# Optimization experiments

Hardware: AMD Instinct MI355X
Metric: run time of the kernel (lower is better)

## Reference

```python
import jax, jax.numpy as jnp
import numpy as np

EMBED_DIM = 1024
NUM_HEADS = 16
HEAD_DIM = EMBED_DIM // NUM_HEADS


def setup_inputs() -> dict:
    key = jax.random.key(0)
    ks = jax.random.split(key, 7)
    B, S, E = 2, 2048, EMBED_DIM
    scale = 1.0 / np.sqrt(E)
    x = jax.random.normal(ks[0], (B, S, E), dtype=jnp.float32)
    Wq = jax.random.normal(ks[1], (E, E), dtype=jnp.float32) * scale
    Wk = jax.random.normal(ks[2], (E, E), dtype=jnp.float32) * scale
    Wv = jax.random.normal(ks[3], (E, E), dtype=jnp.float32) * scale
    bq = jax.random.normal(ks[4], (E,), dtype=jnp.float32) * 0.01
    bk = jax.random.normal(ks[5], (E,), dtype=jnp.float32) * 0.01
    bv = jax.random.normal(ks[6], (E,), dtype=jnp.float32) * 0.01
    return {"x": x, "Wq": Wq, "bq": bq, "Wk": Wk, "bk": bk, "Wv": Wv, "bv": bv}


def reference(x, Wq, bq, Wk, bk, Wv, bv):
    B, S, E = x.shape
    H, D = NUM_HEADS, HEAD_DIM
    # QKV projections (nn.Linear: x @ W^T + b; W sampled square so we use x @ W + b equivalently as the learned map)
    q = (x @ Wq + bq).reshape(B, S, H, D)
    k = (x @ Wk + bk).reshape(B, S, H, D)
    v = (x @ Wv + bv).reshape(B, S, H, D)
    # scores: [B, H, S, S] -- NOTE: original applies no 1/sqrt(d) scaling
    scores = jnp.einsum("bqhd,bkhd->bhqk", q, k)
    attn = jax.nn.softmax(scores, axis=-1)
    out = jnp.einsum("bhqk,bkhd->bqhd", attn, v)
    return out.reshape(B, S, E)
```

## Files before the change

kernel.cpp:

```cpp
#include <hip/hip_runtime.h>

#define E_DIM 1024
#define NHEADS 16
#define HDIM 64
#define BATCH 2
#define SEQ 2048
#define M_TOT (BATCH*SEQ)

typedef _Float16 f16;
typedef _Float16 half4 __attribute__((ext_vector_type(4)));
typedef _Float16 half8 __attribute__((ext_vector_type(8)));
typedef _Float16 half2v __attribute__((ext_vector_type(2)));
typedef float floatx4 __attribute__((ext_vector_type(4)));

#define MFMA16x32(a,b,c) __builtin_amdgcn_mfma_f32_16x16x32_f16((a),(b),(c),0,0,0)
#define EXP2F(x) __builtin_amdgcn_exp2f(x)
#define FMAX3(a,b,c) fmaxf(fmaxf((a),(b)),(c))

__device__ __forceinline__ half2v pkrtz(float a, float b) {
    return __builtin_bit_cast(half2v, __builtin_amdgcn_cvt_pkrtz(a, b));
}

__device__ __forceinline__ void gll16(const f16* gsrc, f16* ldst) {
    __builtin_amdgcn_global_load_lds(
        (const __attribute__((address_space(1))) void*)gsrc,
        (__attribute__((address_space(3))) void*)ldst, 16, 0, 0);
}

__global__ __launch_bounds__(256) void cvt_x(const float* __restrict__ x,
                                             f16* __restrict__ xh) {
    size_t i = ((size_t)blockIdx.x * 256 + threadIdx.x) * 8;
    float4 a = *(const float4*)&x[i];
    float4 b = *(const float4*)&x[i + 4];
    half8 h = {(f16)a.x,(f16)a.y,(f16)a.z,(f16)a.w,
               (f16)b.x,(f16)b.y,(f16)b.z,(f16)b.w};
    *(half8*)&xh[i] = h;
}

__global__ __launch_bounds__(256) void transpose_w(
    const float* __restrict__ Wq, const float* __restrict__ Wk,
    const float* __restrict__ Wv,
    f16* __restrict__ WTq, f16* __restrict__ WTk, f16* __restrict__ WTv)
{
    const int z = blockIdx.z;
    const float* W = (z == 0) ? Wq : (z == 1) ? Wk : Wv;
    f16* WT        = (z == 0) ? WTq : (z == 1) ? WTk : WTv;

    const int k0 = blockIdx.x * 64, n0 = blockIdx.y * 64;
    const int tid = threadIdx.x;
    __shared__ f16 T[64][68];

    {
        const int tr = tid >> 4, tc = tid & 15;
        float4 f4[4];
        #pragma unroll
        for (int i = 0; i < 4; i++)
            f4[i] = *(const float4*)&W[(size_t)(k0 + tr * 4 + i) * E_DIM + n0 + tc * 4];
        #pragma unroll
        for (int j = 0; j < 4; j++) {
            float e0 = (j==0)?f4[0].x:(j==1)?f4[0].y:(j==2)?f4[0].z:f4[0].w;
            float e1 = (j==0)?f4[1].x:(j==1)?f4[1].y:(j==2)?f4[1].z:f4[1].w;
            float e2 = (j==0)?f4[2].x:(j==1)?f4[2].y:(j==2)?f4[2].z:f4[2].w;
            float e3 = (j==0)?f4[3].x:(j==1)?f4[3].y:(j==2)?f4[3].z:f4[3].w;
            half4 h = {(f16)e0, (f16)e1, (f16)e2, (f16)e3};
            *(half4*)&T[tc * 4 + j][tr * 4] = h;
        }
    }
    __syncthreads();
    {
        const int nn = tid >> 2, kk = (tid & 3) * 16;
        half8 a = *(const half8*)&T[nn][kk];
        half8 b = *(const half8*)&T[nn][kk + 8];
        f16* dst = &WT[(size_t)(n0 + nn) * E_DIM + k0 + kk];
        *(half8*)dst = a;
        *(half8*)(dst + 8) = b;
    }
}

__global__ __launch_bounds__(256) void qkv_gemm(
    const f16* __restrict__ xh, const f16* __restrict__ WTall,
    const float* __restrict__ bq, const float* __restrict__ bk,
    const float* __restrict__ bv,
    f16* __restrict__ qh, f16* __restrict__ kh, f16* __restrict__ vh)
{
    const int flat = blockIdx.x;
    const int rb = (flat & 7) * 96 + (flat >> 3);
    const int z   = rb >> 8;
    const int ntl = rb & 7;
    const int mt  = (rb >> 3) & 31;

    const float* bias = (z == 0) ? bq : (z == 1) ? bk : bv;
    f16* out          = (z == 0) ? qh : (z == 1) ? kh : vh;

    const int m0 = mt * 128;
    const int n0g = z * 1024 + ntl * 128;
    const int tid = threadIdx.x;
    const int lane = tid & 63;
    const int w  = tid >> 6;
    const int wm = w >> 1, wn = w & 1;
    const int g  = lane >> 4, r = lane & 15;

    __shared__ f16 Al[128 * 64];
    __shared__ f16 Bl[128 * 64];

    const int lrow = lane >> 3;
    const int lcol = ((lane & 7) ^ lrow) * 8;
    const f16* asrc = xh    + (size_t)(m0  + lrow) * E_DIM + lcol;
    const f16* bsrc = WTall + (size_t)(n0g + lrow) * E_DIM + lcol;

    floatx4 acc[4][4];
    #pragma unroll
    for (int i = 0; i < 4; i++)
        #pragma unroll
        for (int j = 0; j < 4; j++)
            acc[i][j] = (floatx4){0.f, 0.f, 0.f, 0.f};

    for (int k0 = 0; k0 < E_DIM; k0 += 64) {
        if (k0) __syncthreads();
        #pragma unroll
        for (int t = 0; t < 4; t++) {
            int c = w * 4 + t;
            gll16(asrc + (size_t)c * 8 * E_DIM + k0, Al + c * 512);
            gll16(bsrc + (size_t)c * 8 * E_DIM + k0, Bl + c * 512);
        }
        __syncthreads();

        #pragma unroll
        for (int ks = 0; ks < 64; ks += 32) {
            half8 af[4], bf[4];
            #pragma unroll
            for (int i = 0; i < 4; i++) {
                int row = wm * 64 + i * 16 + r;
                af[i] = *(const half8*)&Al[row * 64 + ((ks + g * 8) ^ ((row & 7) << 3))];
            }
            #pragma unroll
            for (int j = 0; j < 4; j++) {
                int row = wn * 64 + j * 16 + r;
                bf[j] = *(const half8*)&Bl[row * 64 + ((ks + g * 8) ^ ((row & 7) << 3))];
            }
            #pragma unroll
            for (int i = 0; i < 4; i++)
                #pragma unroll
                for (int j = 0; j < 4; j++)
                    acc[i][j] = MFMA16x32(af[i], bf[j], acc[i][j]);
        }
    }

    #pragma unroll
    for (int j = 0; j < 4; j++) {
        int col = ntl * 128 + wn * 64 + j * 16 + r;
        float bb = bias[col];
        #pragma unroll
        for (int i = 0; i < 4; i++)
            #pragma unroll
            for (int rr = 0; rr < 4; rr++) {
                int row = m0 + wm * 64 + i * 16 + g * 4 + rr;
                out[(size_t)row * E_DIM + col] = (f16)(acc[i][j][rr] + bb);
            }
    }
}

__global__ __launch_bounds__(256) void qkv_proj_v2(
    const float* __restrict__ x,
    const f16* __restrict__ WTq, const f16* __restrict__ WTk,
    const f16* __restrict__ WTv,
    const float* __restrict__ bq, const float* __restrict__ bk,
    const float* __restrict__ bv,
    f16* __restrict__ qh, f16* __restrict__ kh, f16* __restrict__ vh)
{
    const int flat = blockIdx.x;
    const int rb = (flat & 7) * 96 + (flat >> 3);
    const int nt = rb & 7;
    const int mt = (rb >> 3) & 31;
    const int z  = rb >> 8;

    const f16* WT     = (z == 0) ? WTq : (z == 1) ? WTk : WTv;
    const float* bias = (z == 0) ? bq : (z == 1) ? bk : bv;
    f16* out          = (z == 0) ? qh : (z == 1) ? kh : vh;

    const int m0 = mt * 128, n0 = nt * 128;
    const int tid = threadIdx.x;
    const int lane = tid & 63;
    const int w  = tid >> 6;
    const int wm = w >> 1, wn = w & 1;
    const int g  = lane >> 4, r = lane & 15;

    __shared__ f16 Al[128 * 32];
    __shared__ f16 Bl[128 * 32];

    floatx4 acc[4][4];
    #pragma unroll
    for (int i = 0; i < 4; i++)
        #pragma unroll
        for (int j = 0; j < 4; j++)
            acc[i][j] = (floatx4){0.f, 0.f, 0.f, 0.f};

    for (int k0 = 0; k0 < E_DIM; k0 += 32) {
        #pragma unroll
        for (int it = 0; it < 2; it++) {
            int idx = tid + it * 256;
            int mm = idx >> 2, kc = (idx & 3) * 8;
            const float* s = &x[(size_t)(m0 + mm) * E_DIM + k0 + kc];
            float4 u = *(const float4*)s;
            float4 v = *(const float4*)(s + 4);
            half8 hv = {(f16)u.x,(f16)u.y,(f16)u.z,(f16)u.w,
                        (f16)v.x,(f16)v.y,(f16)v.z,(f16)v.w};
            *(half8*)&Al[mm * 32 + (kc ^ (((mm >> 2) & 3) << 3))] = hv;
        }
        #pragma unroll
        for (int it = 0; it < 2; it++) {
            int idx = tid + it * 256;
            int nn = idx >> 2, kc = (idx & 3) * 8;
            half8 hv = *(const half8*)&WT[(size_t)(n0 + nn) * E_DIM + k0 + kc];
            *(half8*)&Bl[nn * 32 + (kc ^ (((nn >> 2) & 3) << 3))] = hv;
        }
        __syncthreads();

        half8 af[4], bf[4];
        #pragma unroll
        for (int i = 0; i < 4; i++) {
            int row = wm * 64 + i * 16 + r;
            af[i] = *(const half8*)&Al[row * 32 + ((g * 8) ^ (((row >> 2) & 3) << 3))];
        }
        #pragma unroll
        for (int j = 0; j < 4; j++) {
            int row = wn * 64 + j * 16 + r;
            bf[j] = *(const half8*)&Bl[row * 32 + ((g * 8) ^ (((row >> 2) & 3) << 3))];
        }
        #pragma unroll
        for (int i = 0; i < 4; i++)
            #pragma unroll
            for (int j = 0; j < 4; j++)
                acc[i][j] = MFMA16x32(af[i], bf[j], acc[i][j]);
        __syncthreads();
    }

    #pragma unroll
    for (int j = 0; j < 4; j++) {
        int col = n0 + wn * 64 + j * 16 + r;
        float bb = bias[col];
        #pragma unroll
        for (int i = 0; i < 4; i++)
            #pragma unroll
            for (int rr = 0; rr < 4; rr++) {
                int row = m0 + wm * 64 + i * 16 + g * 4 + rr;
                out[(size_t)row * E_DIM + col] = (f16)(acc[i][j][rr] + bb);
            }
    }
}

__global__ __launch_bounds__(512, 4) void attn(
    const f16* __restrict__ qh, const f16* __restrict__ kh,
    const f16* __restrict__ vh, float* __restrict__ out)
{
    const int flat = blockIdx.x;
    const int rb = (flat & 7) * 64 + (flat >> 3);
    const int qt = rb & 15;
    const int hh = (rb >> 4) & 15;
    const int b  = rb >> 8;
    const int q0 = qt * 128;

    const int tid = threadIdx.x;
    const int lane = tid & 63;
    const int w = tid >> 6;
    const int g = lane >> 4, r = lane & 15;

    __shared__ f16 K_s[2][64 * 64];
    __shared__ f16 V_s[2][64 * 64];

    const size_t base = ((size_t)b * SEQ) * E_DIM + (size_t)hh * HDIM;

    half8 aq[2];
    {
        const f16* qp = &qh[base + (size_t)(q0 + w * 16 + r) * E_DIM];
        aq[0] = *(const half8*)&qp[g * 8] * (f16)1.44269504f;
        aq[1] = *(const half8*)&qp[32 + g * 8] * (f16)1.44269504f;
    }

    const int klrow = lane >> 3;
    const int kcol = ((lane & 7) ^ klrow) * 8;
    const f16* kg0 = kh + base + (size_t)(w * 8 + klrow) * E_DIM + kcol;

    const int vp = tid >> 4, vdc = (tid & 15) * 4;
    const int kv0 = vp * 2;
    const int kvp0 = (kv0 & 3) | (((kv0 >> 4) & 1) << 2) |
                     (((kv0 >> 2) & 3) << 3) | ((kv0 >> 5) << 5);
    const f16* vg0 = vh + base + (size_t)kv0 * E_DIM + vdc;
    int voff[4];
    #pragma unroll
    for (int e = 0; e < 4; e++) {
        int d = vdc + e;
        voff[e] = d * 64 + (kvp0 ^ (((d ^ (d >> 3)) & 7) << 3));
    }

    const half8 ones = {(f16)1.f,(f16)1.f,(f16)1.f,(f16)1.f,
                        (f16)1.f,(f16)1.f,(f16)1.f,(f16)1.f};

    float m_run = -1e30f;
    floatx4 acco[4];
    floatx4 acc5 = (floatx4){0.f, 0.f, 0.f, 0.f};
    #pragma unroll
    for (int dj = 0; dj < 4; dj++) acco[dj] = (floatx4){0.f, 0.f, 0.f, 0.f};

    const int NT = SEQ / 64;

    gll16(kg0, &K_s[0][w * 512]);
    {
        half4 v0 = *(const half4*)vg0;
        half4 v1 = *(const half4*)(vg0 + E_DIM);
        #pragma unroll
        for (int e = 0; e < 4; e++) {
            half2v pr = {v0[e], v1[e]};
            *(half2v*)&V_s[0][voff[e]] = pr;
        }
    }
    __syncthreads();

    for (int t = 0; t < NT; t++) {
        const int cur = t & 1;
        const bool pf = (t + 1 < NT);
        half4 v0n, v1n;
        if (pf) {
            gll16(kg0 + (size_t)(t + 1) * 64 * E_DIM, &K_s[cur ^ 1][w * 512]);
            const f16* vsrc = vg0 + (size_t)(t + 1) * 64 * E_DIM;
            v0n = *(const half4*)vsrc;
            v1n = *(const half4*)(vsrc + E_DIM);
        }

        floatx4 sct[4];
        __builtin_amdgcn_s_setprio(1);
        #pragma unroll
        for (int kb = 0; kb < 4; kb++) {
            int kr2 = kb * 16 + r;
            int swk = (kr2 & 7) << 3;
            const f16* kb_ = &K_s[cur][kr2 * 64];
            half8 kf0 = *(const half8*)&kb_[(g * 8) ^ swk];
            half8 kf1 = *(const half8*)&kb_[(32 + g * 8) ^ swk];
            floatx4 c = (floatx4){0.f, 0.f, 0.f, 0.f};
            c = MFMA16x32(kf0, aq[0], c);
            c = MFMA16x32(kf1, aq[1], c);
            sct[kb] = c;
        }
        __builtin_amdgcn_s_setprio(0);

        float t0 = FMAX3(sct[0][0], sct[0][1], sct[0][2]);
        float t1 = FMAX3(sct[0][3], sct[1][0], sct[1][1]);
        float t2 = FMAX3(sct[1][2], sct[1][3], sct[2][0]);
        float t3 = FMAX3(sct[2][1], sct[2][2], sct[2][3]);
        float t4 = FMAX3(sct[3][0], sct[3][1], sct[3][2]);
        float pm = fmaxf(FMAX3(t0, t1, t2), FMAX3(t3, t4, sct[3][3]));
        pm = fmaxf(pm, __shfl_xor(pm, 16, 64));
        pm = fmaxf(pm, __shfl_xor(pm, 32, 64));
        if (!__all(pm - m_run <= 11.544f)) {
            float mn = fmaxf(m_run, pm);
            float alpha = EXP2F(m_run - mn);
            m_run = mn;
            acc5 *= alpha;
            #pragma unroll
            for (int dj = 0; dj < 4; dj++)
                #pragma unroll
                for (int rr = 0; rr < 4; rr++)
                    acco[dj][rr] *= alpha;
        }

        union H8 { half8 v; half2v h2[4]; };
        half8 pa[2];
        #pragma unroll
        for (int h = 0; h < 2; h++) {
            H8 u;
            #pragma unroll
            for (int q = 0; q < 2; q++) {
                int kb = h * 2 + q;
                u.h2[q * 2 + 0] = pkrtz(
                    EXP2F(sct[kb][0] - m_run), EXP2F(sct[kb][1] - m_run));
                u.h2[q * 2 + 1] = pkrtz(
                    EXP2F(sct[kb][2] - m_run), EXP2F(sct[kb][3] - m_run));
            }
            pa[h] = u.v;
        }

        if (pf) {
            #pragma unroll
            for (int e = 0; e < 4; e++) {
                half2v pr = {v0n[e], v1n[e]};
                *(half2v*)&V_s[cur ^ 1][voff[e]] = pr;
            }
        }

        __builtin_amdgcn_s_setprio(1);
        #pragma unroll
        for (int dj = 0; dj < 4; dj++) {
            int d = dj * 16 + r;
            int swv = ((d ^ (d >> 3)) & 7) << 3;
            const f16* vb_ = &V_s[cur][d * 64];
            half8 vf0 = *(const half8*)&vb_[(g * 8) ^ swv];
            half8 vf1 = *(const half8*)&vb_[(32 + g * 8) ^ swv];
            acco[dj] = MFMA16x32(vf0, pa[0], acco[dj]);
            acco[dj] = MFMA16x32(vf1, pa[1], acco[dj]);
        }
        acc5 = MFMA16x32(ones, pa[0], acc5);
        acc5 = MFMA16x32(ones, pa[1], acc5);
        __builtin_amdgcn_s_setprio(0);

        __syncthreads();
    }

    {
        float inv = 1.f / acc5[0];
        int row = q0 + w * 16 + r;
        float* orow = out + (size_t)(b * SEQ + row) * E_DIM + hh * HDIM;
        #pragma unroll
        for (int dj = 0; dj < 4; dj++) {
            float4 st = {acco[dj][0] * inv, acco[dj][1] * inv,
                         acco[dj][2] * inv, acco[dj][3] * inv};
            *(float4*)&orow[dj * 16 + g * 4] = st;
        }
    }
}

extern "C" void kernel_launch(void* const* d_in, const int* in_sizes, int n_in,
                              void* d_out, int out_size, void* d_ws, size_t ws_size,
                              hipStream_t stream) {
    const float* x  = (const float*)d_in[0];
    const float* Wq = (const float*)d_in[1];
    const float* bq = (const float*)d_in[2];
    const float* Wk = (const float*)d_in[3];
    const float* bk = (const float*)d_in[4];
    const float* Wv = (const float*)d_in[5];
    const float* bv = (const float*)d_in[6];
    float* out = (float*)d_out;

    const size_t qkv_elems = (size_t)M_TOT * E_DIM;
    const size_t w_elems   = (size_t)E_DIM * E_DIM;
    f16* qh  = (f16*)d_ws;
    f16* kh  = qh + qkv_elems;
    f16* vh  = kh + qkv_elems;
    f16* WTq = vh + qkv_elems;
    f16* WTk = WTq + w_elems;
    f16* WTv = WTk + w_elems;
    f16* xh  = WTv + w_elems;
    const size_t need_v3  = (3 * qkv_elems + 3 * w_elems + qkv_elems) * sizeof(f16);
    const size_t need_v2  = (3 * qkv_elems + 3 * w_elems) * sizeof(f16);
    if (ws_size < need_v2) return;

    if (ws_size >= need_v3) {
        cvt_x<<<dim3(M_TOT * E_DIM / (256 * 8)), 256, 0, stream>>>(x, xh);
        transpose_w<<<dim3(16, 16, 3), 256, 0, stream>>>(Wq, Wk, Wv, WTq, WTk, WTv);
        qkv_gemm<<<dim3((E_DIM / 128) * (M_TOT / 128) * 3), 256, 0, stream>>>(
            xh, WTq, bq, bk, bv, qh, kh, vh);
    } else {
        transpose_w<<<dim3(16, 16, 3), 256, 0, stream>>>(Wq, Wk, Wv, WTq, WTk, WTv);
        qkv_proj_v2<<<dim3((E_DIM / 128) * (M_TOT / 128) * 3), 256, 0, stream>>>(
            x, WTq, WTk, WTv, bq, bk, bv, qh, kh, vh);
    }
    attn<<<dim3((SEQ / 128) * NHEADS * BATCH), 512, 0, stream>>>(qh, kh, vh, out);
}
```

Measured before the change: 169.1 us.

## Software-pipeline QK^T one tile ahead in attention and merge prep kernels

The attention loop now computes the QK^T scores for tile t+1 while the softmax and PV work for tile t is in flight. It keeps two score register sets and unrolls the loop by two, so K/V global loads are issued two tiles ahead. The x-conversion and weight-transpose kernels are merged into one launch, which saves a kernel launch. The fallback GEMM path for small workspaces is removed. The extra live score registers may raise register pressure under launch_bounds(512,4).

```diff
diff --git a/kernel.cpp b/kernel.cpp
--- a/kernel.cpp
+++ b/kernel.cpp
@@ -27,29 +27,29 @@
         (__attribute__((address_space(3))) void*)ldst, 16, 0, 0);
 }
 
-__global__ __launch_bounds__(256) void cvt_x(const float* __restrict__ x,
-                                             f16* __restrict__ xh) {
-    size_t i = ((size_t)blockIdx.x * 256 + threadIdx.x) * 8;
-    float4 a = *(const float4*)&x[i];
-    float4 b = *(const float4*)&x[i + 4];
-    half8 h = {(f16)a.x,(f16)a.y,(f16)a.z,(f16)a.w,
-               (f16)b.x,(f16)b.y,(f16)b.z,(f16)b.w};
-    *(half8*)&xh[i] = h;
-}
-
-__global__ __launch_bounds__(256) void transpose_w(
+__global__ __launch_bounds__(256) void prep(
+    const float* __restrict__ x, f16* __restrict__ xh,
     const float* __restrict__ Wq, const float* __restrict__ Wk,
     const float* __restrict__ Wv,
     f16* __restrict__ WTq, f16* __restrict__ WTk, f16* __restrict__ WTv)
 {
-    const int z = blockIdx.z;
+    const int tid = threadIdx.x;
+    if (blockIdx.x < 2048) {
+        size_t i = ((size_t)blockIdx.x * 256 + tid) * 8;
+        float4 a = *(const float4*)&x[i];
+        float4 b = *(const float4*)&x[i + 4];
+        half8 h = {(f16)a.x,(f16)a.y,(f16)a.z,(f16)a.w,
+                   (f16)b.x,(f16)b.y,(f16)b.z,(f16)b.w};
+        *(half8*)&xh[i] = h;
+        return;
+    }
+    const int f = blockIdx.x - 2048;
+    const int z = f >> 8;
+    const int k0 = (f & 15) * 64, n0 = ((f >> 4) & 15) * 64;
     const float* W = (z == 0) ? Wq : (z == 1) ? Wk : Wv;
     f16* WT        = (z == 0) ? WTq : (z == 1) ? WTk : WTv;
 
-    const int k0 = blockIdx.x * 64, n0 = blockIdx.y * 64;
-    const int tid = threadIdx.x;
     __shared__ f16 T[64][68];
-
     {
         const int tr = tid >> 4, tc = tid & 15;
         float4 f4[4];
@@ -160,95 +160,6 @@
     }
 }
 
-__global__ __launch_bounds__(256) void qkv_proj_v2(
-    const float* __restrict__ x,
-    const f16* __restrict__ WTq, const f16* __restrict__ WTk,
-    const f16* __restrict__ WTv,
-    const float* __restrict__ bq, const float* __restrict__ bk,
-    const float* __restrict__ bv,
-    f16* __restrict__ qh, f16* __restrict__ kh, f16* __restrict__ vh)
-{
-    const int flat = blockIdx.x;
-    const int rb = (flat & 7) * 96 + (flat >> 3);
-    const int nt = rb & 7;
-    const int mt = (rb >> 3) & 31;
-    const int z  = rb >> 8;
-
-    const f16* WT     = (z == 0) ? WTq : (z == 1) ? WTk : WTv;
-    const float* bias = (z == 0) ? bq : (z == 1) ? bk : bv;
-    f16* out          = (z == 0) ? qh : (z == 1) ? kh : vh;
-
-    const int m0 = mt * 128, n0 = nt * 128;
-    const int tid = threadIdx.x;
-    const int lane = tid & 63;
-    const int w  = tid >> 6;
-    const int wm = w >> 1, wn = w & 1;
-    const int g  = lane >> 4, r = lane & 15;
-
-    __shared__ f16 Al[128 * 32];
-    __shared__ f16 Bl[128 * 32];
-
-    floatx4 acc[4][4];
-    #pragma unroll
-    for (int i = 0; i < 4; i++)
-        #pragma unroll
-        for (int j = 0; j < 4; j++)
-            acc[i][j] = (floatx4){0.f, 0.f, 0.f, 0.f};
-
-    for (int k0 = 0; k0 < E_DIM; k0 += 32) {
-        #pragma unroll
-        for (int it = 0; it < 2; it++) {
-            int idx = tid + it * 256;
-            int mm = idx >> 2, kc = (idx & 3) * 8;
-            const float* s = &x[(size_t)(m0 + mm) * E_DIM + k0 + kc];
-            float4 u = *(const float4*)s;
-            float4 v = *(const float4*)(s + 4);
-            half8 hv = {(f16)u.x,(f16)u.y,(f16)u.z,(f16)u.w,
-                        (f16)v.x,(f16)v.y,(f16)v.z,(f16)v.w};
-            *(half8*)&Al[mm * 32 + (kc ^ (((mm >> 2) & 3) << 3))] = hv;
-        }
-        #pragma unroll
-        for (int it = 0; it < 2; it++) {
-            int idx = tid + it * 256;
-            int nn = idx >> 2, kc = (idx & 3) * 8;
-            half8 hv = *(const half8*)&WT[(size_t)(n0 + nn) * E_DIM + k0 + kc];
-            *(half8*)&Bl[nn * 32 + (kc ^ (((nn >> 2) & 3) << 3))] = hv;
-        }
-        __syncthreads();
-
-        half8 af[4], bf[4];
-        #pragma unroll
-        for (int i = 0; i < 4; i++) {
-            int row = wm * 64 + i * 16 + r;
-            af[i] = *(const half8*)&Al[row * 32 + ((g * 8) ^ (((row >> 2) & 3) << 3))];
-        }
-        #pragma unroll
-        for (int j = 0; j < 4; j++) {
-            int row = wn * 64 + j * 16 + r;
-            bf[j] = *(const half8*)&Bl[row * 32 + ((g * 8) ^ (((row >> 2) & 3) << 3))];
-        }
-        #pragma unroll
-        for (int i = 0; i < 4; i++)
-            #pragma unroll
-            for (int j = 0; j < 4; j++)
-                acc[i][j] = MFMA16x32(af[i], bf[j], acc[i][j]);
-        __syncthreads();
-    }
-
-    #pragma unroll
-    for (int j = 0; j < 4; j++) {
-        int col = n0 + wn * 64 + j * 16 + r;
-        float bb = bias[col];
-        #pragma unroll
-        for (int i = 0; i < 4; i++)
-            #pragma unroll
-            for (int rr = 0; rr < 4; rr++) {
-                int row = m0 + wm * 64 + i * 16 + g * 4 + rr;
-                out[(size_t)row * E_DIM + col] = (f16)(acc[i][j][rr] + bb);
-            }
-    }
-}
-
 __global__ __launch_bounds__(512, 4) void attn(
     const f16* __restrict__ qh, const f16* __restrict__ kh,
     const f16* __restrict__ vh, float* __restrict__ out)
@@ -304,6 +215,9 @@
 
     const int NT = SEQ / 64;
 
+    floatx4 sA[4], sB[4];
+    half4 vP0, vP1, vQ0, vQ1;
+
     gll16(kg0, &K_s[0][w * 512]);
     {
         half4 v0 = *(const half4*)vg0;
@@ -315,95 +229,121 @@
         }
     }
     __syncthreads();
-
-    for (int t = 0; t < NT; t++) {
-        const int cur = t & 1;
-        const bool pf = (t + 1 < NT);
-        half4 v0n, v1n;
-        if (pf) {
-            gll16(kg0 + (size_t)(t + 1) * 64 * E_DIM, &K_s[cur ^ 1][w * 512]);
-            const f16* vsrc = vg0 + (size_t)(t + 1) * 64 * E_DIM;
-            v0n = *(const half4*)vsrc;
-            v1n = *(const half4*)(vsrc + E_DIM);
-        }
-
-        floatx4 sct[4];
-        __builtin_amdgcn_s_setprio(1);
-        #pragma unroll
-        for (int kb = 0; kb < 4; kb++) {
-            int kr2 = kb * 16 + r;
-            int swk = (kr2 & 7) << 3;
-            const f16* kb_ = &K_s[cur][kr2 * 64];
-            half8 kf0 = *(const half8*)&kb_[(g * 8) ^ swk];
-            half8 kf1 = *(const half8*)&kb_[(32 + g * 8) ^ swk];
-            floatx4 c = (floatx4){0.f, 0.f, 0.f, 0.f};
-            c = MFMA16x32(kf0, aq[0], c);
-            c = MFMA16x32(kf1, aq[1], c);
-            sct[kb] = c;
-        }
-        __builtin_amdgcn_s_setprio(0);
-
-        float t0 = FMAX3(sct[0][0], sct[0][1], sct[0][2]);
-        float t1 = FMAX3(sct[0][3], sct[1][0], sct[1][1]);
-        float t2 = FMAX3(sct[1][2], sct[1][3], sct[2][0]);
-        float t3 = FMAX3(sct[2][1], sct[2][2], sct[2][3]);
-        float t4 = FMAX3(sct[3][0], sct[3][1], sct[3][2]);
-        float pm = fmaxf(FMAX3(t0, t1, t2), FMAX3(t3, t4, sct[3][3]));
-        pm = fmaxf(pm, __shfl_xor(pm, 16, 64));
-        pm = fmaxf(pm, __shfl_xor(pm, 32, 64));
-        if (!__all(pm - m_run <= 11.544f)) {
-            float mn = fmaxf(m_run, pm);
-            float alpha = EXP2F(m_run - mn);
-            m_run = mn;
-            acc5 *= alpha;
-            #pragma unroll
-            for (int dj = 0; dj < 4; dj++)
-                #pragma unroll
-                for (int rr = 0; rr < 4; rr++)
-                    acco[dj][rr] *= alpha;
-        }
-
-        union H8 { half8 v; half2v h2[4]; };
+    #pragma unroll
+    for (int kb = 0; kb < 4; kb++) {
+        int kr2 = kb * 16 + r;
+        int swk = (kr2 & 7) << 3;
+        const f16* kb_ = &K_s[0][kr2 * 64];
+        half8 kf0 = *(const half8*)&kb_[(g * 8) ^ swk];
+        half8 kf1 = *(const half8*)&kb_[(32 + g * 8) ^ swk];
+        floatx4 c = (floatx4){0.f, 0.f, 0.f, 0.f};
+        c = MFMA16x32(kf0, aq[0], c);
+        c = MFMA16x32(kf1, aq[1], c);
+        sA[kb] = c;
+    }
+    gll16(kg0 + (size_t)64 * E_DIM, &K_s[1][w * 512]);
+    {
+        const f16* vsrc = vg0 + (size_t)64 * E_DIM;
+        vP0 = *(const half4*)vsrc;
+        vP1 = *(const half4*)(vsrc + E_DIM);
+    }
+    __syncthreads();
+
+#define ATTN_ITER(T, SC, SN, VW0, VW1, VL0, VL1, CUR)                          \
+    do {                                                                       \
+                                             \
+        if ((T) + 1 < NT) {                                                    \
+            _Pragma("unroll")                                                  \
+            for (int kb = 0; kb < 4; kb++) {                                   \
+                int kr2 = kb * 16 + r;                                         \
+                int swk = (kr2 & 7) << 3;                                      \
+                const f16* kb_ = &K_s[(CUR) ^ 1][kr2 * 64];                    \
+                half8 kf0 = *(const half8*)&kb_[(g * 8) ^ swk];                \
+                half8 kf1 = *(const half8*)&kb_[(32 + g * 8) ^ swk];           \
+                floatx4 c = (floatx4){0.f, 0.f, 0.f, 0.f};                     \
+                c = MFMA16x32(kf0, aq[0], c);                                  \
+                c = MFMA16x32(kf1, aq[1], c);                                  \
+                SN[kb] = c;                                                    \
+            }                                                                  \
+        }                                                                      \
+                                            \
+        if ((T) + 2 < NT)                                                      \
+            gll16(kg0 + (size_t)((T) + 2) * 64 * E_DIM, &K_s[CUR][w * 512]);   \
+                          \
+        {                                                                      \
+            float t0 = FMAX3(SC[0][0], SC[0][1], SC[0][2]);                    \
+            float t1 = FMAX3(SC[0][3], SC[1][0], SC[1][1]);                    \
+            float t2 = FMAX3(SC[1][2], SC[1][3], SC[2][0]);                    \
+            float t3 = FMAX3(SC[2][1], SC[2][2], SC[2][3]);                    \
+            float t4 = FMAX3(SC[3][0], SC[3][1], SC[3][2]);                    \
+            float pm = fmaxf(FMAX3(t0, t1, t2), FMAX3(t3, t4, SC[3][3]));      \
+            pm = fmaxf(pm, __shfl_xor(pm, 16, 64));                            \
+            pm = fmaxf(pm, __shfl_xor(pm, 32, 64));                            \
+            if (!__all(pm - m_run <= 11.544f)) {                               \
+                float mn = fmaxf(m_run, pm);                                   \
+                float alpha = EXP2F(m_run - mn);                               \
+                m_run = mn;                                                    \
+                acc5 *= alpha;                                                 \
+                _Pragma("unroll")                                              \
+                for (int dj = 0; dj < 4; dj++)                                 \
+                    _Pragma("unroll")                                          \
+                    for (int rr = 0; rr < 4; rr++)                             \
+                        acco[dj][rr] *= alpha;                                 \
+            }                                                                  \
+        }                                                                      \
+        {                                                                      \
+            union H8 { half8 v; half2v h2[4]; };                               \
+            _Pragma("unroll")                                                  \
+            for (int h = 0; h < 2; h++) {                                      \
+                H8 u;                                                          \
+                _Pragma("unroll")                                              \
+                for (int q = 0; q < 2; q++) {                                  \
+                    int kb = h * 2 + q;                                        \
+                    u.h2[q * 2 + 0] = pkrtz(EXP2F(SC[kb][0] - m_run),          \
+                                            EXP2F(SC[kb][1] - m_run));         \
+                    u.h2[q * 2 + 1] = pkrtz(EXP2F(SC[kb][2] - m_run),          \
+                                            EXP2F(SC[kb][3] - m_run));         \
+                }                                                              \
+                pa[h] = u.v;                                                   \
+            }                                                                  \
+        }                                                                      \
+                             \
+        if ((T) + 1 < NT) {                                                    \
+            _Pragma("unroll")                                                  \
+            for (int e = 0; e < 4; e++) {                                      \
+                half2v pr = {VW0[e], VW1[e]};                                  \
+                *(half2v*)&V_s[(CUR) ^ 1][voff[e]] = pr;                       \
+            }                                                                  \
+        }                                                                      \
+        if ((T) + 2 < NT) {                                                    \
+            const f16* vsrc = vg0 + (size_t)((T) + 2) * 64 * E_DIM;            \
+            VL0 = *(const half4*)vsrc;                                         \
+            VL1 = *(const half4*)(vsrc + E_DIM);                               \
+        }                                                                      \
+                                            \
+        __builtin_amdgcn_s_setprio(1);                                         \
+        _Pragma("unroll")                                                      \
+        for (int dj = 0; dj < 4; dj++) {                                       \
+            int d = dj * 16 + r;                                               \
+            int swv = ((d ^ (d >> 3)) & 7) << 3;                               \
+            const f16* vb_ = &V_s[CUR][d * 64];                                \
+            half8 vf0 = *(const half8*)&vb_[(g * 8) ^ swv];                    \
+            half8 vf1 = *(const half8*)&vb_[(32 + g * 8) ^ swv];               \
+            acco[dj] = MFMA16x32(vf0, pa[0], acco[dj]);                        \
+            acco[dj] = MFMA16x32(vf1, pa[1], acco[dj]);                        \
+        }                                                                      \
+        acc5 = MFMA16x32(ones, pa[0], acc5);                                   \
+        acc5 = MFMA16x32(ones, pa[1], acc5);                                   \
+        __builtin_amdgcn_s_setprio(0);                                         \
+        __syncthreads();                                                       \
+    } while (0)
+
+    for (int t = 0; t < NT; t += 2) {
         half8 pa[2];
-        #pragma unroll
-        for (int h = 0; h < 2; h++) {
-            H8 u;
-            #pragma unroll
-            for (int q = 0; q < 2; q++) {
-                int kb = h * 2 + q;
-                u.h2[q * 2 + 0] = pkrtz(
-                    EXP2F(sct[kb][0] - m_run), EXP2F(sct[kb][1] - m_run));
-                u.h2[q * 2 + 1] = pkrtz(
-                    EXP2F(sct[kb][2] - m_run), EXP2F(sct[kb][3] - m_run));
-            }
-            pa[h] = u.v;
-        }
-
-        if (pf) {
-            #pragma unroll
-            for (int e = 0; e < 4; e++) {
-                half2v pr = {v0n[e], v1n[e]};
-                *(half2v*)&V_s[cur ^ 1][voff[e]] = pr;
-            }
-        }
-
-        __builtin_amdgcn_s_setprio(1);
-        #pragma unroll
-        for (int dj = 0; dj < 4; dj++) {
-            int d = dj * 16 + r;
-            int swv = ((d ^ (d >> 3)) & 7) << 3;
-            const f16* vb_ = &V_s[cur][d * 64];
-            half8 vf0 = *(const half8*)&vb_[(g * 8) ^ swv];
-            half8 vf1 = *(const half8*)&vb_[(32 + g * 8) ^ swv];
-            acco[dj] = MFMA16x32(vf0, pa[0], acco[dj]);
-            acco[dj] = MFMA16x32(vf1, pa[1], acco[dj]);
-        }
-        acc5 = MFMA16x32(ones, pa[0], acc5);
-        acc5 = MFMA16x32(ones, pa[1], acc5);
-        __builtin_amdgcn_s_setprio(0);
-
-        __syncthreads();
-    }
+        ATTN_ITER(t,     sA, sB, vP0, vP1, vQ0, vQ1, 0);
+        ATTN_ITER(t + 1, sB, sA, vQ0, vQ1, vP0, vP1, 1);
+    }
+#undef ATTN_ITER
 
     {
         float inv = 1.f / acc5[0];
@@ -439,19 +379,11 @@
     f16* WTk = WTq + w_elems;
     f16* WTv = WTk + w_elems;
     f16* xh  = WTv + w_elems;
-    const size_t need_v3  = (3 * qkv_elems + 3 * w_elems + qkv_elems) * sizeof(f16);
-    const size_t need_v2  = (3 * qkv_elems + 3 * w_elems) * sizeof(f16);
-    if (ws_size < need_v2) return;
-
-    if (ws_size >= need_v3) {
-        cvt_x<<<dim3(M_TOT * E_DIM / (256 * 8)), 256, 0, stream>>>(x, xh);
-        transpose_w<<<dim3(16, 16, 3), 256, 0, stream>>>(Wq, Wk, Wv, WTq, WTk, WTv);
-        qkv_gemm<<<dim3((E_DIM / 128) * (M_TOT / 128) * 3), 256, 0, stream>>>(
-            xh, WTq, bq, bk, bv, qh, kh, vh);
-    } else {
-        transpose_w<<<dim3(16, 16, 3), 256, 0, stream>>>(Wq, Wk, Wv, WTq, WTk, WTv);
-        qkv_proj_v2<<<dim3((E_DIM / 128) * (M_TOT / 128) * 3), 256, 0, stream>>>(
-            x, WTq, WTk, WTv, bq, bk, bv, qh, kh, vh);
-    }
+    const size_t need = (4 * qkv_elems + 3 * w_elems) * sizeof(f16);
+    if (ws_size < need) return;
+
+    prep<<<dim3(2048 + 768), 256, 0, stream>>>(x, xh, Wq, Wk, Wv, WTq, WTk, WTv);
+    qkv_gemm<<<dim3((E_DIM / 128) * (M_TOT / 128) * 3), 256, 0, stream>>>(
+        xh, WTq, bq, bk, bv, qh, kh, vh);
     attn<<<dim3((SEQ / 128) * NHEADS * BATCH), 512, 0, stream>>>(qh, kh, vh, out);
 }
```

Result: faster. 163.0 us (-3.6%).
